# Performance work log

Hardware: AMD Instinct MI355X
Metric: run time of the kernel (lower is better)

Reference implementation:

```python
import jax, jax.numpy as jnp
import numpy as np

# Sobel kernels stacked as [O=2, I=1, 3, 3]
_KX = np.array([[-1., 0., 1.], [-2., 0., 2.], [-1., 0., 1.]], dtype=np.float32)
_KY = np.array([[1., 2., 1.], [0., 0., 0.], [-1., -2., -1.]], dtype=np.float32)
_SOBEL_W = jnp.asarray(np.stack([_KX, _KY])[:, None, :, :])  # [2,1,3,3]


def _sobel(x):
    # x: [B,1,H,W] -> |Gx| + |Gy| : [B,1,H,W]
    g = jax.lax.conv_general_dilated(
        x, _SOBEL_W, window_strides=(1, 1), padding=((1, 1), (1, 1)),
        dimension_numbers=('NCHW', 'OIHW', 'NCHW'))  # [B,2,H,W]
    return jnp.sum(jnp.abs(g), axis=1, keepdims=True)


def _threshold_mask(g, k):
    # g: [B,1,H,W]; k-th SMALLEST over flattened (C*H*W) per batch (torch.kthvalue)
    B, N, H, W = g.shape
    flat = g.reshape(B, N, H * W)
    kth = jnp.sort(flat, axis=-1)[:, :, k - 1:k]  # [B,N,1]
    mask = (flat >= kth).astype(g.dtype)
    return mask.reshape(B, N, H, W)


def setup_inputs() -> dict:
    key = jax.random.key(0)
    kA, kB, kF = jax.random.split(key, 3)
    shape = (8, 3, 1024, 1024)
    return {
        'image_A': jax.random.uniform(kA, shape, dtype=jnp.float32),
        'image_B': jax.random.uniform(kB, shape, dtype=jnp.float32),
        'image_fused': jax.random.uniform(kF, shape, dtype=jnp.float32),
        'thresholds': 524288,
    }


def reference(image_A, image_B, image_fused, thresholds):
    gA = _sobel(image_A[:, :1])
    gB = _sobel(image_B[:, :1])
    gF = _sobel(image_fused[:, :1])
    joint_max = jnp.maximum(gA, gB)  # max over concat([gA,gB], dim=1) with 1 ch each
    maskA = _threshold_mask(gA, thresholds)
    maskB = _threshold_mask(gB, thresholds)
    loss = jnp.mean(jnp.abs(gF - joint_max))
    return (loss, maskA, maskB)
```

## Files before the change

kernel.cpp:

```cpp
#include <hip/hip_runtime.h>

#define IMG_H 1024
#define IMG_W 1024
#define NBATCH 8
#define NCH 3
#define NPIX (IMG_H * IMG_W)
#define NTOT (8388608LL)

#define BINS1 4096
#define SH1 19

#define SEGS 64
#define ROWS_PER_SEG 16

#define WS_MISC_OFF   0
#define WS_H1R_OFF    4096
#define WS_H1R_BYTES  (2 * NBATCH * BINS1 * 4)
#define WS_LOSSP_OFF  (WS_H1R_OFF + WS_H1R_BYTES)
#define WS_LOSSP_BYTES (NBATCH * SEGS * 8)
#define WS_LIST_OFF   (WS_LOSSP_OFF + WS_LOSSP_BYTES)

struct Row3f { float l, c, r; };

__device__ __forceinline__ Row3f load3(const float* __restrict__ img, int y, int x) {
    Row3f o;
    if ((unsigned)y >= (unsigned)IMG_H) { o.l = o.c = o.r = 0.0f; return o; }
    const float* row = img + (size_t)y * IMG_W;
    o.c = row[x];
    o.l = (x > 0)         ? row[x - 1] : 0.0f;
    o.r = (x < IMG_W - 1) ? row[x + 1] : 0.0f;
    return o;
}

__device__ __forceinline__ float sobel_g(const Row3f& r0, const Row3f& r1, const Row3f& r2) {
    float gx = r0.r - r0.l;
    gx -= 2.0f * r1.l;
    gx += 2.0f * r1.r;
    gx -= r2.l;
    gx += r2.r;
    float gy = r0.l + 2.0f * r0.c;
    gy += r0.r;
    gy -= r2.l;
    gy -= 2.0f * r2.c;
    gy -= r2.r;
    return fabsf(gx) + fabsf(gy);
}

__device__ __forceinline__ unsigned wave_scan(unsigned s, int lane) {
    #pragma unroll
    for (int off = 1; off < 64; off <<= 1) {
        const unsigned v = __shfl_up(s, off);
        if (lane >= off) s += v;
    }
    return s;
}

extern "C" __global__ __launch_bounds__(1024)
void k_pass0(const float* __restrict__ A, const float* __restrict__ B,
             const float* __restrict__ F,
             unsigned int* __restrict__ hist1r, double* __restrict__ lossPart)
{
    __shared__ unsigned int h[4 * BINS1];
    __shared__ double lsum[16];
    const int t = threadIdx.x;
    const int lane = t & 63;
    for (int i = t; i < 4 * BINS1; i += 1024) h[i] = 0u;
    __syncthreads();

    const int blk = blockIdx.x;
    const int batch = blk >> 6;
    const int y0 = (blk & 63) * ROWS_PER_SEG;
    const int x = t;
    unsigned int* hc = h + (t >> 9) * (2 * BINS1);

    const float* a = A + (size_t)batch * NCH * NPIX;
    const float* b = B + (size_t)batch * NCH * NPIX;
    const float* f = F + (size_t)batch * NCH * NPIX;

    Row3f a0 = load3(a, y0 - 1, x), a1 = load3(a, y0, x), a2;
    Row3f b0 = load3(b, y0 - 1, x), b1 = load3(b, y0, x), b2;
    Row3f f0 = load3(f, y0 - 1, x), f1 = load3(f, y0, x), f2;

    double loss = 0.0;
    for (int i = 0; i < ROWS_PER_SEG; ++i) {
        const int y = y0 + i;
        a2 = load3(a, y + 1, x);
        b2 = load3(b, y + 1, x);
        f2 = load3(f, y + 1, x);
        const float gA = sobel_g(a0, a1, a2);
        const float gB = sobel_g(b0, b1, b2);
        const float gF = sobel_g(f0, f1, f2);
        atomicAdd(&hc[__float_as_uint(gA) >> SH1], 1u);
        atomicAdd(&hc[BINS1 + (__float_as_uint(gB) >> SH1)], 1u);
        loss += (double)fabsf(gF - fmaxf(gA, gB));
        a0 = a1; a1 = a2;
        b0 = b1; b1 = b2;
        f0 = f1; f1 = f2;
    }
    __syncthreads();

    for (int i = t; i < 2 * BINS1; i += 1024) {
        const unsigned v = h[i] + h[2 * BINS1 + i];
        if (v) {
            unsigned int* dst = (i < BINS1)
                ? &hist1r[(size_t)batch * BINS1 + i]
                : &hist1r[(size_t)(NBATCH + batch) * BINS1 + (i - BINS1)];
            atomicAdd(dst, v);
        }
    }

    for (int off = 32; off > 0; off >>= 1) loss += __shfl_down(loss, off);
    if (lane == 0) lsum[t >> 6] = loss;
    __syncthreads();
    if (t == 0) {
        double s = 0.0;
        for (int i = 0; i < 16; ++i) s += lsum[i];
        lossPart[blk] = s;
    }
}

extern "C" __global__ __launch_bounds__(1024)
void k_select1(const unsigned int* __restrict__ hist1r, const double* __restrict__ lossPart,
               const int* __restrict__ kptr, int* __restrict__ sel1, int* __restrict__ resid1,
               double* __restrict__ lossAcc, unsigned int* __restrict__ gCnt)
{
    const int ib = blockIdx.x, t = threadIdx.x;
    const int lane = t & 63, wid = t >> 6;

    long long kl = (long long)kptr[0];
    if (kl < 1 || kl > (long long)NPIX) {
        float kf = ((const float*)kptr)[0];
        kl = (long long)kf;
        if (kl < 1) kl = 1;
        if (kl > NPIX) kl = NPIX;
    }
    const unsigned k = (unsigned)kl;

    const uint4 c = ((const uint4*)(hist1r + (size_t)ib * BINS1))[t];
    const unsigned s = c.x + c.y + c.z + c.w;

    unsigned incl = wave_scan(s, lane);
    __shared__ unsigned wsum[16];
    __shared__ double dsum[16];
    if (lane == 63) wsum[wid] = incl;
    __syncthreads();
    if (wid == 0) {
        unsigned w = (lane < 16) ? wsum[lane] : 0u;
        w = wave_scan(w, lane);
        if (lane < 16) wsum[lane] = w;
    }
    __syncthreads();
    if (wid > 0) incl += wsum[wid - 1];

    const unsigned excl = incl - s;
    if (excl < k && k <= incl) {
        unsigned cum = excl; int bin = t * 4;
        if (cum + c.x < k) { cum += c.x; ++bin;
          if (cum + c.y < k) { cum += c.y; ++bin;
            if (cum + c.z < k) { cum += c.z; ++bin; } } }
        sel1[ib] = bin;
        resid1[ib] = (int)(k - cum);
    }

    double v = 0.0;
    if (ib == 0 && t < NBATCH * SEGS) v = lossPart[t];
    for (int off = 32; off > 0; off >>= 1) v += __shfl_down(v, off);
    if (lane == 0) dsum[wid] = v;
    __syncthreads();
    if (ib == 0 && t == 0) {
        double sL = 0.0;
        for (int i = 0; i < 16; ++i) sL += dsum[i];
        lossAcc[0] = sL;
    }
    if (t == 0) gCnt[ib] = 0u;
}

extern "C" __global__ __launch_bounds__(1024)
void k_passB(const float* __restrict__ A, const float* __restrict__ B,
             const int* __restrict__ sel1, unsigned int* __restrict__ gCnt,
             uint2* __restrict__ list, unsigned cap, float* __restrict__ out)
{
    const int t = threadIdx.x;
    const int blk = blockIdx.x;
    const int batch = blk >> 6;
    const int y0 = (blk & 63) * ROWS_PER_SEG;
    const int x = t;

    const float* a = A + (size_t)batch * NCH * NPIX;
    const float* b = B + (size_t)batch * NCH * NPIX;
    const unsigned sA = (unsigned)sel1[batch];
    const unsigned sB = (unsigned)sel1[NBATCH + batch];
    float* mA = out + 1 + (size_t)batch * NPIX;
    float* mB = out + 1 + (size_t)NTOT + (size_t)batch * NPIX;

    __shared__ uint2 bufA[2048], bufB[2048];
    __shared__ unsigned cntA, cntB, baseA, baseB;
    if (t == 0) { cntA = 0u; cntB = 0u; }
    __syncthreads();

    Row3f a0 = load3(a, y0 - 1, x), a1 = load3(a, y0, x), a2;
    Row3f b0 = load3(b, y0 - 1, x), b1 = load3(b, y0, x), b2;
    for (int i = 0; i < ROWS_PER_SEG; ++i) {
        const int y = y0 + i;
        a2 = load3(a, y + 1, x);
        b2 = load3(b, y + 1, x);
        const unsigned uA = __float_as_uint(sobel_g(a0, a1, a2));
        const unsigned uB = __float_as_uint(sobel_g(b0, b1, b2));
        const unsigned binA = uA >> SH1, binB = uB >> SH1;
        const unsigned idx = (unsigned)y * IMG_W + (unsigned)x;
        mA[idx] = (binA > sA) ? 1.0f : 0.0f;
        mB[idx] = (binB > sB) ? 1.0f : 0.0f;
        if (binA == sA) { unsigned p = atomicAdd(&cntA, 1u); bufA[p] = make_uint2(uA, idx); }
        if (binB == sB) { unsigned p = atomicAdd(&cntB, 1u); bufB[p] = make_uint2(uB, idx); }
        a0 = a1; a1 = a2;
        b0 = b1; b1 = b2;

        __syncthreads();
        const bool last = (i == ROWS_PER_SEG - 1);
        const unsigned nA = cntA, nB = cntB;
        const bool doA = (nA >= 1024u) || (last && nA > 0u);
        const bool doB = (nB >= 1024u) || (last && nB > 0u);
        if (doA || doB) {
            if (t == 0) {
                if (doA) baseA = atomicAdd(&gCnt[batch], nA);
                if (doB) baseB = atomicAdd(&gCnt[NBATCH + batch], nB);
            }
            __syncthreads();
            if (doA) {
                const unsigned bs = baseA;
                for (unsigned j = t; j < nA; j += 1024u) {
                    const unsigned d = bs + j;
                    if (d < cap) list[(size_t)batch * cap + d] = bufA[j];
                }
            }
            if (doB) {
                const unsigned bs = baseB;
                for (unsigned j = t; j < nB; j += 1024u) {
                    const unsigned d = bs + j;
                    if (d < cap) list[(size_t)(NBATCH + batch) * cap + d] = bufB[j];
                }
            }
            __syncthreads();
            if (t == 0) { if (doA) cntA = 0u; if (doB) cntB = 0u; }
        }
        __syncthreads();
    }
}

extern "C" __global__ __launch_bounds__(1024)
void k_selectfix(const uint2* __restrict__ list, const unsigned int* __restrict__ gCnt,
                 unsigned cap, const int* __restrict__ sel1, const int* __restrict__ resid1,
                 const double* __restrict__ lossAcc, float* __restrict__ out)
{
    const int ib = blockIdx.x, t = threadIdx.x;
    const int lane = t & 63, wid = t >> 6;
    unsigned n = gCnt[ib]; if (n > cap) n = cap;
    const unsigned kk = (unsigned)resid1[ib];
    const uint2* L = list + (size_t)ib * cap;

    __shared__ unsigned h2[BINS1];
    __shared__ unsigned wsum[16];
    __shared__ unsigned bcast[4];
    if (t < 4) bcast[t] = 0u;
    for (int i = t; i < BINS1; i += 1024) h2[i] = 0u;
    __syncthreads();

    for (unsigned j = t; j < n; j += 1024u) atomicAdd(&h2[(L[j].x >> 7) & 4095u], 1u);
    __syncthreads();

    const unsigned c0 = h2[4 * t], c1 = h2[4 * t + 1], c2 = h2[4 * t + 2], c3 = h2[4 * t + 3];
    const unsigned s = c0 + c1 + c2 + c3;
    unsigned incl = wave_scan(s, lane);
    if (lane == 63) wsum[wid] = incl;
    __syncthreads();
    if (wid == 0) {
        unsigned w = (lane < 16) ? wsum[lane] : 0u;
        w = wave_scan(w, lane);
        if (lane < 16) wsum[lane] = w;
    }
    __syncthreads();
    if (wid > 0) incl += wsum[wid - 1];
    {
        const unsigned excl = incl - s;
        if (excl < kk && kk <= incl) {
            unsigned cum = excl; unsigned bin = 4u * t;
            if (cum + c0 < kk) { cum += c0; ++bin;
              if (cum + c1 < kk) { cum += c1; ++bin;
                if (cum + c2 < kk) { cum += c2; ++bin; } } }
            bcast[0] = bin;
            bcast[1] = kk - cum;
        }
    }
    __syncthreads();
    const unsigned sel2 = bcast[0], k3 = bcast[1];

    if (t < 128) h2[t] = 0u;
    __syncthreads();
    for (unsigned j = t; j < n; j += 1024u) {
        const unsigned bbits = L[j].x;
        if (((bbits >> 7) & 4095u) == sel2) atomicAdd(&h2[bbits & 127u], 1u);
    }
    __syncthreads();
    {
        const unsigned s3 = (t < 128) ? h2[t] : 0u;
        unsigned incl3 = wave_scan(s3, lane);
        if (lane == 63) wsum[wid] = incl3;
        __syncthreads();
        if (wid == 0) {
            unsigned w = (lane < 16) ? wsum[lane] : 0u;
            w = wave_scan(w, lane);
            if (lane < 16) wsum[lane] = w;
        }
        __syncthreads();
        if (wid > 0) incl3 += wsum[wid - 1];
        const unsigned excl3 = incl3 - s3;
        if (t < 128 && excl3 < k3 && k3 <= incl3) {
            bcast[2] = ((unsigned)sel1[ib] << SH1) | (sel2 << 7) | (unsigned)t;
        }
    }
    __syncthreads();
    const unsigned kth = bcast[2];

    float* m = out + 1 + (size_t)ib * NPIX;
    for (unsigned j = t; j < n; j += 1024u) {
        const uint2 e = L[j];
        m[e.y] = (e.x >= kth) ? 1.0f : 0.0f;
    }
    if (ib == 0 && t == 0) out[0] = (float)(lossAcc[0] * (1.0 / 8388608.0));
}

extern "C" void kernel_launch(void* const* d_in, const int* in_sizes, int n_in,
                              void* d_out, int out_size, void* d_ws, size_t ws_size,
                              hipStream_t stream)
{
    const float* A = (const float*)d_in[0];
    const float* B = (const float*)d_in[1];
    const float* F = (const float*)d_in[2];
    const int* kptr = (const int*)d_in[3];
    float* out = (float*)d_out;

    if (ws_size < (size_t)WS_LIST_OFF + 16 * 8 * 1024) return;

    char* ws = (char*)d_ws;
    double* lossAcc        = (double*)(ws + WS_MISC_OFF);
    unsigned int* gCnt     = (unsigned int*)(ws + WS_MISC_OFF + 64);
    int* sel1              = (int*)(ws + WS_MISC_OFF + 128);
    int* resid1            = (int*)(ws + WS_MISC_OFF + 256);
    unsigned int* hist1r   = (unsigned int*)(ws + WS_H1R_OFF);
    double* lossPart       = (double*)(ws + WS_LOSSP_OFF);
    uint2* list            = (uint2*)(ws + WS_LIST_OFF);

    unsigned long long capll = (ws_size - WS_LIST_OFF) / (16ull * 8ull);
    unsigned cap = (capll > (unsigned long long)NPIX) ? (unsigned)NPIX : (unsigned)capll;

    hipMemsetAsync(ws + WS_H1R_OFF, 0, WS_H1R_BYTES, stream);

    k_pass0    <<<dim3(NBATCH * SEGS), dim3(1024), 0, stream>>>(A, B, F, hist1r, lossPart);
    k_select1  <<<dim3(2 * NBATCH), dim3(1024), 0, stream>>>(hist1r, lossPart, kptr, sel1, resid1, lossAcc, gCnt);
    k_passB    <<<dim3(NBATCH * SEGS), dim3(1024), 0, stream>>>(A, B, sel1, gCnt, list, cap, out);
    k_selectfix<<<dim3(2 * NBATCH), dim3(1024), 0, stream>>>(list, gCnt, cap, sel1, resid1, lossAcc, out);
}
```

Baseline: 322.5 us.

## Fuse sobel, histogram select and mask passes into one cooperative kernel

```diff
diff --git a/kernel.cpp b/kernel.cpp
--- a/kernel.cpp
+++ b/kernel.cpp
@@ -1,4 +1,7 @@
 #include <hip/hip_runtime.h>
+#include <hip/hip_cooperative_groups.h>
+
+namespace cg = cooperative_groups;
 
 #define IMG_H 1024
 #define IMG_W 1024
@@ -10,6 +13,8 @@
 #define BINS1 4096
 #define SH1 19
 
+#define FB_BLOCKS 256
+#define FB_ROWS 32
 #define SEGS 64
 #define ROWS_PER_SEG 16
 
@@ -17,7 +22,7 @@
 #define WS_H1R_OFF    4096
 #define WS_H1R_BYTES  (2 * NBATCH * BINS1 * 4)
 #define WS_LOSSP_OFF  (WS_H1R_OFF + WS_H1R_BYTES)
-#define WS_LOSSP_BYTES (NBATCH * SEGS * 8)
+#define WS_LOSSP_BYTES 4096
 #define WS_LIST_OFF   (WS_LOSSP_OFF + WS_LOSSP_BYTES)
 
 struct Row3f { float l, c, r; };
@@ -53,6 +58,303 @@
         if (lane >= off) s += v;
     }
     return s;
+}
+
+__device__ __forceinline__ void ast_u32(unsigned* p, unsigned v) {
+    __hip_atomic_store(p, v, __ATOMIC_RELAXED, __HIP_MEMORY_SCOPE_AGENT);
+}
+__device__ __forceinline__ unsigned ald_u32(const unsigned* p) {
+    return __hip_atomic_load(p, __ATOMIC_RELAXED, __HIP_MEMORY_SCOPE_AGENT);
+}
+__device__ __forceinline__ void ast_u64(unsigned long long* p, unsigned long long v) {
+    __hip_atomic_store(p, v, __ATOMIC_RELAXED, __HIP_MEMORY_SCOPE_AGENT);
+}
+__device__ __forceinline__ unsigned long long ald_u64(const unsigned long long* p) {
+    return __hip_atomic_load(p, __ATOMIC_RELAXED, __HIP_MEMORY_SCOPE_AGENT);
+}
+__device__ __forceinline__ unsigned long long pack64(unsigned bits, unsigned idx) {
+    return (unsigned long long)bits | ((unsigned long long)idx << 32);
+}
+
+extern "C" __global__ __launch_bounds__(1024, 4)
+void k_fused(const float* __restrict__ A, const float* __restrict__ B,
+             const float* __restrict__ F, const int* __restrict__ kptr,
+             float* __restrict__ out,
+             unsigned* __restrict__ hist1r, unsigned long long* __restrict__ lossPart,
+             unsigned* __restrict__ gCnt, unsigned* __restrict__ sel1,
+             unsigned* __restrict__ resid1, unsigned long long* __restrict__ list,
+             unsigned cap)
+{
+    cg::grid_group grid = cg::this_grid();
+
+    __shared__ unsigned h[4 * BINS1];
+    __shared__ double lsum[16];
+    __shared__ double dsum[16];
+    __shared__ unsigned wsum[16];
+    __shared__ unsigned bcast[4];
+    __shared__ unsigned cntA, cntB, baseA, baseB;
+
+    const int blk = blockIdx.x;
+    const int t = threadIdx.x;
+    const int lane = t & 63, wid = t >> 6;
+    const int batch = blk >> 5;
+    const int y0 = (blk & 31) * FB_ROWS;
+    const int x = t;
+
+    {
+        const int idx = blk * 1024 + t;
+        if (idx < 2 * NBATCH * BINS1) ast_u32(&hist1r[idx], 0u);
+        if (blk == 0 && t < 16) ast_u32(&gCnt[t], 0u);
+    }
+    __threadfence();
+    grid.sync();
+
+    for (int i = t; i < 4 * BINS1; i += 1024) h[i] = 0u;
+    __syncthreads();
+
+    unsigned* hc = h + (t >> 9) * (2 * BINS1);
+
+    const float* a = A + (size_t)batch * NCH * NPIX;
+    const float* b = B + (size_t)batch * NCH * NPIX;
+    const float* f = F + (size_t)batch * NCH * NPIX;
+
+    unsigned uAr[FB_ROWS], uBr[FB_ROWS];
+
+    {
+        Row3f a0 = load3(a, y0 - 1, x), a1 = load3(a, y0, x), a2;
+        Row3f b0 = load3(b, y0 - 1, x), b1 = load3(b, y0, x), b2;
+        Row3f f0 = load3(f, y0 - 1, x), f1 = load3(f, y0, x), f2;
+        double loss = 0.0;
+        #pragma unroll
+        for (int i = 0; i < FB_ROWS; ++i) {
+            const int y = y0 + i;
+            a2 = load3(a, y + 1, x);
+            b2 = load3(b, y + 1, x);
+            f2 = load3(f, y + 1, x);
+            const float gA = sobel_g(a0, a1, a2);
+            const float gB = sobel_g(b0, b1, b2);
+            const float gF = sobel_g(f0, f1, f2);
+            const unsigned uA = __float_as_uint(gA), uB = __float_as_uint(gB);
+            uAr[i] = uA; uBr[i] = uB;
+            atomicAdd(&hc[uA >> SH1], 1u);
+            atomicAdd(&hc[BINS1 + (uB >> SH1)], 1u);
+            loss += (double)fabsf(gF - fmaxf(gA, gB));
+            a0 = a1; a1 = a2;
+            b0 = b1; b1 = b2;
+            f0 = f1; f1 = f2;
+        }
+        __syncthreads();
+
+        for (int i = t; i < 2 * BINS1; i += 1024) {
+            const unsigned v = h[i] + h[2 * BINS1 + i];
+            if (v) {
+                unsigned* dst = (i < BINS1)
+                    ? &hist1r[(size_t)batch * BINS1 + i]
+                    : &hist1r[(size_t)(NBATCH + batch) * BINS1 + (i - BINS1)];
+                atomicAdd(dst, v);
+            }
+        }
+
+        for (int off = 32; off > 0; off >>= 1) loss += __shfl_down(loss, off);
+        if (lane == 0) lsum[wid] = loss;
+        __syncthreads();
+        if (t == 0) {
+            double s = 0.0;
+            for (int i = 0; i < 16; ++i) s += lsum[i];
+            ast_u64(&lossPart[blk], (unsigned long long)__double_as_longlong(s));
+        }
+    }
+    __threadfence();
+    grid.sync();
+
+    double lossTotal = 0.0;
+    if (blk < 16) {
+        const int ib = blk;
+        long long kl = (long long)kptr[0];
+        if (kl < 1 || kl > (long long)NPIX) {
+            float kf = ((const float*)kptr)[0];
+            kl = (long long)kf;
+            if (kl < 1) kl = 1;
+            if (kl > NPIX) kl = NPIX;
+        }
+        const unsigned k = (unsigned)kl;
+
+        const unsigned* hr = hist1r + (size_t)ib * BINS1 + 4 * t;
+        const unsigned c0 = ald_u32(hr + 0), c1 = ald_u32(hr + 1);
+        const unsigned c2 = ald_u32(hr + 2), c3 = ald_u32(hr + 3);
+        const unsigned s = c0 + c1 + c2 + c3;
+
+        unsigned incl = wave_scan(s, lane);
+        if (lane == 63) wsum[wid] = incl;
+        __syncthreads();
+        if (wid == 0) {
+            unsigned w = (lane < 16) ? wsum[lane] : 0u;
+            w = wave_scan(w, lane);
+            if (lane < 16) wsum[lane] = w;
+        }
+        __syncthreads();
+        if (wid > 0) incl += wsum[wid - 1];
+
+        const unsigned excl = incl - s;
+        if (excl < k && k <= incl) {
+            unsigned cum = excl; unsigned bin = (unsigned)t * 4u;
+            if (cum + c0 < k) { cum += c0; ++bin;
+              if (cum + c1 < k) { cum += c1; ++bin;
+                if (cum + c2 < k) { cum += c2; ++bin; } } }
+            ast_u32(&sel1[ib], bin);
+            ast_u32(&resid1[ib], k - cum);
+        }
+    }
+    if (blk == 0) {
+        double v = 0.0;
+        if (t < FB_BLOCKS) v = __longlong_as_double((long long)ald_u64(&lossPart[t]));
+        for (int off = 32; off > 0; off >>= 1) v += __shfl_down(v, off);
+        if (lane == 0) dsum[wid] = v;
+        __syncthreads();
+        if (t == 0) {
+            double s = 0.0;
+            for (int i = 0; i < 16; ++i) s += dsum[i];
+            lossTotal = s;
+        }
+    }
+    __threadfence();
+    grid.sync();
+
+    {
+        const unsigned sA = ald_u32(&sel1[batch]);
+        const unsigned sB = ald_u32(&sel1[NBATCH + batch]);
+        float* mA = out + 1 + (size_t)batch * NPIX;
+        float* mB = out + 1 + (size_t)NTOT + (size_t)batch * NPIX;
+        unsigned long long* LA = list + (size_t)batch * cap;
+        unsigned long long* LB = list + (size_t)(NBATCH + batch) * cap;
+        unsigned long long* bufA = (unsigned long long*)h;
+        unsigned long long* bufB = ((unsigned long long*)h) + 2048;
+
+        if (t == 0) { cntA = 0u; cntB = 0u; }
+        __syncthreads();
+
+        #pragma unroll
+        for (int i = 0; i < FB_ROWS; ++i) {
+            const unsigned uA = uAr[i], uB = uBr[i];
+            const unsigned binA = uA >> SH1, binB = uB >> SH1;
+            const unsigned idx = (unsigned)(y0 + i) * IMG_W + (unsigned)x;
+            mA[idx] = (binA > sA) ? 1.0f : 0.0f;
+            mB[idx] = (binB > sB) ? 1.0f : 0.0f;
+            if (binA == sA) { unsigned p = atomicAdd(&cntA, 1u); bufA[p] = pack64(uA, idx); }
+            if (binB == sB) { unsigned p = atomicAdd(&cntB, 1u); bufB[p] = pack64(uB, idx); }
+
+            __syncthreads();
+            const bool last = (i == FB_ROWS - 1);
+            const unsigned nA = cntA, nB = cntB;
+            const bool doA = (nA >= 1024u) || (last && nA > 0u);
+            const bool doB = (nB >= 1024u) || (last && nB > 0u);
+            if (doA || doB) {
+                if (t == 0) {
+                    if (doA) baseA = atomicAdd(&gCnt[batch], nA);
+                    if (doB) baseB = atomicAdd(&gCnt[NBATCH + batch], nB);
+                }
+                __syncthreads();
+                if (doA) {
+                    const unsigned bs = baseA;
+                    for (unsigned j = t; j < nA; j += 1024u) {
+                        const unsigned d = bs + j;
+                        if (d < cap) ast_u64(&LA[d], bufA[j]);
+                    }
+                }
+                if (doB) {
+                    const unsigned bs = baseB;
+                    for (unsigned j = t; j < nB; j += 1024u) {
+                        const unsigned d = bs + j;
+                        if (d < cap) ast_u64(&LB[d], bufB[j]);
+                    }
+                }
+                __syncthreads();
+                if (t == 0) { if (doA) cntA = 0u; if (doB) cntB = 0u; }
+            }
+            __syncthreads();
+        }
+    }
+    __threadfence();
+    grid.sync();
+    __threadfence();
+
+    if (blk < 16) {
+        const int ib = blk;
+        unsigned n = ald_u32(&gCnt[ib]); if (n > cap) n = cap;
+        const unsigned kk = ald_u32(&resid1[ib]);
+        const unsigned long long* L = list + (size_t)ib * cap;
+        unsigned* h2 = h;
+
+        if (t < 4) bcast[t] = 0u;
+        for (int i = t; i < BINS1; i += 1024) h2[i] = 0u;
+        __syncthreads();
+
+        for (unsigned j = t; j < n; j += 1024u) {
+            const unsigned bits = (unsigned)ald_u64(&L[j]);
+            atomicAdd(&h2[(bits >> 7) & 4095u], 1u);
+        }
+        __syncthreads();
+
+        const unsigned c0 = h2[4 * t], c1 = h2[4 * t + 1], c2 = h2[4 * t + 2], c3 = h2[4 * t + 3];
+        const unsigned s = c0 + c1 + c2 + c3;
+        unsigned incl = wave_scan(s, lane);
+        if (lane == 63) wsum[wid] = incl;
+        __syncthreads();
+        if (wid == 0) {
+            unsigned w = (lane < 16) ? wsum[lane] : 0u;
+            w = wave_scan(w, lane);
+            if (lane < 16) wsum[lane] = w;
+        }
+        __syncthreads();
+        if (wid > 0) incl += wsum[wid - 1];
+        {
+            const unsigned excl = incl - s;
+            if (excl < kk && kk <= incl) {
+                unsigned cum = excl; unsigned bin = 4u * (unsigned)t;
+                if (cum + c0 < kk) { cum += c0; ++bin;
+                  if (cum + c1 < kk) { cum += c1; ++bin;
+                    if (cum + c2 < kk) { cum += c2; ++bin; } } }
+                bcast[0] = bin;
+                bcast[1] = kk - cum;
+            }
+        }
+        __syncthreads();
+        const unsigned sel2 = bcast[0], k3 = bcast[1];
+
+        if (t < 128) h2[t] = 0u;
+        __syncthreads();
+        for (unsigned j = t; j < n; j += 1024u) {
+            const unsigned bits = (unsigned)ald_u64(&L[j]);
+            if (((bits >> 7) & 4095u) == sel2) atomicAdd(&h2[bits & 127u], 1u);
+        }
+        __syncthreads();
+        {
+            const unsigned s3 = (t < 128) ? h2[t] : 0u;
+            unsigned incl3 = wave_scan(s3, lane);
+            if (lane == 63) wsum[wid] = incl3;
+            __syncthreads();
+            if (wid == 0) {
+                unsigned w = (lane < 16) ? wsum[lane] : 0u;
+                w = wave_scan(w, lane);
+                if (lane < 16) wsum[lane] = w;
+            }
+            __syncthreads();
+            if (wid > 0) incl3 += wsum[wid - 1];
+            const unsigned excl3 = incl3 - s3;
+            if (t < 128 && excl3 < k3 && k3 <= incl3) {
+                bcast[2] = (ald_u32(&sel1[ib]) << SH1) | (sel2 << 7) | (unsigned)t;
+            }
+        }
+        __syncthreads();
+        const unsigned kth = bcast[2];
+
+        float* m = out + 1 + (size_t)ib * NPIX;
+        for (unsigned j = t; j < n; j += 1024u) {
+            const unsigned long long e = ald_u64(&L[j]);
+            m[(unsigned)(e >> 32)] = ((unsigned)e >= kth) ? 1.0f : 0.0f;
+        }
+        if (ib == 0 && t == 0) out[0] = (float)(lossTotal * (1.0 / 8388608.0));
+    }
 }
 
 extern "C" __global__ __launch_bounds__(1024)
@@ -353,8 +655,23 @@
     unsigned long long capll = (ws_size - WS_LIST_OFF) / (16ull * 8ull);
     unsigned cap = (capll > (unsigned long long)NPIX) ? (unsigned)NPIX : (unsigned)capll;
 
+    {
+        unsigned* sel1u = (unsigned*)sel1;
+        unsigned* resid1u = (unsigned*)resid1;
+        unsigned long long* lossPart64 = (unsigned long long*)lossPart;
+        unsigned long long* list64 = (unsigned long long*)list;
+        void* kargs[] = {
+            (void*)&A, (void*)&B, (void*)&F, (void*)&kptr, (void*)&out,
+            (void*)&hist1r, (void*)&lossPart64, (void*)&gCnt,
+            (void*)&sel1u, (void*)&resid1u, (void*)&list64, (void*)&cap
+        };
+        hipError_t e = hipLaunchCooperativeKernel((const void*)k_fused,
+                                                  dim3(FB_BLOCKS), dim3(1024),
+                                                  kargs, 0, stream);
+        if (e == hipSuccess) return;
+    }
+
     hipMemsetAsync(ws + WS_H1R_OFF, 0, WS_H1R_BYTES, stream);
-
     k_pass0    <<<dim3(NBATCH * SEGS), dim3(1024), 0, stream>>>(A, B, F, hist1r, lossPart);
     k_select1  <<<dim3(2 * NBATCH), dim3(1024), 0, stream>>>(hist1r, lossPart, kptr, sel1, resid1, lossAcc, gCnt);
     k_passB    <<<dim3(NBATCH * SEGS), dim3(1024), 0, stream>>>(A, B, sel1, gCnt, list, cap, out);
```

Result: slower. 902.7 us (+179.9%).
